# Optimization experiments

Measured on AMD Instinct MI355X. Metric: run time of the kernel, lower is better.

The kernel has to match this reference:

```python
import jax, jax.numpy as jnp
import numpy as np

D_MODEL, D_K, D_V, H_HEADS = 512, 64, 64, 8
HH, WW = 28, 28
LN_EPS = 1e-5


def setup_inputs() -> dict:
    key = jax.random.key(0)
    ks = jax.random.split(key, 20)
    b, nq, nk = 64, HH * WW, (HH // 2) * (WW // 2)
    def xavier(k, shape):
        fan_in, fan_out = shape[1], shape[0]
        std = float(np.sqrt(2.0 / (fan_in + fan_out)))
        return jax.random.normal(k, shape, jnp.float32) * std
    return {
        "queries": jax.random.normal(ks[0], (b, nq, D_MODEL), jnp.float32),
        "keys": jax.random.normal(ks[1], (b, nk, D_MODEL), jnp.float32),
        "values": jax.random.normal(ks[2], (b, nk, D_MODEL), jnp.float32),
        "Wq": xavier(ks[3], (H_HEADS * D_K, D_MODEL)), "bq": jnp.zeros((H_HEADS * D_K,), jnp.float32),
        "Wk": xavier(ks[4], (H_HEADS * D_K, D_MODEL)), "bk": jnp.zeros((H_HEADS * D_K,), jnp.float32),
        "Wv": xavier(ks[5], (H_HEADS * D_V, D_MODEL)), "bv": jnp.zeros((H_HEADS * D_V,), jnp.float32),
        "Wo": xavier(ks[6], (D_MODEL, H_HEADS * D_V)), "bo": jnp.zeros((D_MODEL,), jnp.float32),
        # depthwise 1x1 stride-2 conv: per-channel scale + bias
        "sr_w": xavier(ks[7], (D_MODEL, 1)).reshape(D_MODEL),
        "sr_b": jnp.zeros((D_MODEL,), jnp.float32),
        "ln_w": jnp.ones((D_MODEL,), jnp.float32), "ln_b": jnp.zeros((D_MODEL,), jnp.float32),
        # 1x1 conv mixing the head dim of attention scores
        "tw": xavier(ks[8], (H_HEADS, H_HEADS)), "tb": jnp.zeros((H_HEADS,), jnp.float32),
    }


def reference(queries, keys, values, Wq, bq, Wk, bk, Wv, bv, Wo, bo,
              sr_w, sr_b, ln_w, ln_b, tw, tb):
    b_s, nq, c = queries.shape
    # Q projection -> [b, h, nq, d_k]
    q = (jnp.einsum('bnc,oc->bno', queries, Wq) + bq).reshape(b_s, nq, H_HEADS, D_K).transpose(0, 2, 1, 3)
    # spatial reduction: depthwise 1x1 stride-2 conv == strided subsample * w + b
    x = queries.transpose(0, 2, 1).reshape(b_s, c, HH, WW)
    x = x[:, :, ::2, ::2] * sr_w[None, :, None, None] + sr_b[None, :, None, None]
    x = x.reshape(b_s, c, -1).transpose(0, 2, 1)  # [b, nk, c]
    # LayerNorm over channel dim
    mu = jnp.mean(x, axis=-1, keepdims=True)
    var = jnp.mean(jnp.square(x - mu), axis=-1, keepdims=True)
    x = (x - mu) * jax.lax.rsqrt(var + LN_EPS) * ln_w + ln_b
    nk = x.shape[1]
    k = (jnp.einsum('bnc,oc->bno', x, Wk) + bk).reshape(b_s, nk, H_HEADS, D_K)
    v = (jnp.einsum('bnc,oc->bno', x, Wv) + bv).reshape(b_s, nk, H_HEADS, D_V).transpose(0, 2, 1, 3)
    # attention scores [b, h, nq, nk]
    att = jnp.einsum('bhqd,bkhd->bhqk', q, k) / jnp.sqrt(jnp.float32(D_K))
    # transform: 1x1 conv across heads, then softmax over keys
    att = jnp.einsum('bhqk,gh->bgqk', att, tw) + tb[None, :, None, None]
    att = jax.nn.softmax(att, axis=-1)
    out = jnp.einsum('bhqk,bhkd->bhqd', att, v).transpose(0, 2, 1, 3).reshape(b_s, nq, H_HEADS * D_V)
    out = jnp.einsum('bno,co->bnc', out, Wo) + bo
    return out
```

## Files before the change

kernel.cpp:

```cpp
#include <hip/hip_runtime.h>
#include <stdint.h>

typedef unsigned short u16;
typedef unsigned int   u32;
typedef __attribute__((ext_vector_type(8))) __bf16 bf16x8;
typedef __attribute__((ext_vector_type(4))) float  f32x4;
typedef __attribute__((ext_vector_type(4))) short  s16x4;

#define NB  64
#define NQ  784
#define NK  196
#define NKP 208
#define DM  512

static __device__ inline u16 f2bf(float f) {
  u32 u = __float_as_uint(f);
  u32 r = (u + 0x7fffu + ((u >> 16) & 1u)) >> 16;
  return (u16)r;
}

static __device__ inline bf16x8 ld8(const u16* p) {
  return *reinterpret_cast<const bf16x8*>(p);
}
static __device__ inline f32x4 mfma16(bf16x8 a, bf16x8 b, f32x4 c) {
  return __builtin_amdgcn_mfma_f32_16x16x32_bf16(a, b, c, 0, 0, 0);
}
static __device__ inline f32x4 mfma16k16(s16x4 a, s16x4 b, f32x4 c) {
#if __has_builtin(__builtin_amdgcn_mfma_f32_16x16x16bf16_1k)
  return __builtin_amdgcn_mfma_f32_16x16x16bf16_1k(a, b, c, 0, 0, 0);
#elif __has_builtin(__builtin_amdgcn_mfma_f32_16x16x16_bf16)
  typedef __attribute__((ext_vector_type(4))) __bf16 bf16x4_t;
  union { s16x4 s; bf16x4_t b; } ua, ub;
  ua.s = a; ub.s = b;
  return __builtin_amdgcn_mfma_f32_16x16x16_bf16(ua.b, ub.b, c, 0, 0, 0);
#else
  asm volatile("v_mfma_f32_16x16x16_bf16 %0, %1, %2, %0\n\ts_nop 7\n\ts_nop 7"
               : "+v"(c) : "v"(a), "v"(b));
  return c;
#endif
}

static __device__ inline float sgpr_f(float x) {
  return __uint_as_float(__builtin_amdgcn_readfirstlane(__float_as_uint(x)));
}

static __device__ inline void gl_lds16(const void* g, void* l) {
  __builtin_amdgcn_global_load_lds(
      (const __attribute__((address_space(1))) void*)g,
      (__attribute__((address_space(3))) void*)l, 16, 0, 0);
}

__global__ __launch_bounds__(256) void cvt4_kernel(const float* __restrict__ Wq,
                                                   const float* __restrict__ Wk,
                                                   const float* __restrict__ Wv,
                                                   const float* __restrict__ Wo,
                                                   u16* __restrict__ oq,
                                                   u16* __restrict__ ok,
                                                   u16* __restrict__ ov,
                                                   u16* __restrict__ oo) {
  int sel = blockIdx.x >> 8;
  int blk = blockIdx.x & 255;
  const float* in = (sel == 0) ? Wq : (sel == 1) ? Wk : (sel == 2) ? Wv : Wo;
  u16* out = (sel == 0) ? oq : (sel == 1) ? ok : (sel == 2) ? ov : oo;
  int i = (blk * 256 + threadIdx.x) * 4;
  float4 f = *reinterpret_cast<const float4*>(in + i);
  ushort4 o;
  o.x = f2bf(f.x); o.y = f2bf(f.y); o.z = f2bf(f.z); o.w = f2bf(f.w);
  *reinterpret_cast<ushort4*>(out + i) = o;
}

__global__ __launch_bounds__(256) void cvtln_kernel(const float* __restrict__ q,
                                                    const float* __restrict__ sr_w,
                                                    const float* __restrict__ sr_b,
                                                    const float* __restrict__ ln_w,
                                                    const float* __restrict__ ln_b,
                                                    u16* __restrict__ qbf,
                                                    u16* __restrict__ xln) {
  int w = blockIdx.x * 4 + (threadIdx.x >> 6);
  int lane = threadIdx.x & 63;
  if (w >= NB * NQ) {
    int w2 = w - NB * NQ;
    if (w2 < NB * 12) {
      int b = w2 / 12, pr = w2 % 12;
      u16* outp = xln + ((size_t)(b * NKP + NK + pr)) * DM;
      *reinterpret_cast<uint4*>(outp + lane * 8) = make_uint4(0u, 0u, 0u, 0u);
    }
    return;
  }
  int b = w / NQ, n = w % NQ;
  const float* row = q + ((size_t)w) * DM;
  int c0 = lane * 4, c1 = 256 + lane * 4;
  float4 x0 = *reinterpret_cast<const float4*>(row + c0);
  float4 x1 = *reinterpret_cast<const float4*>(row + c1);
  u16* qp = qbf + (size_t)w * DM;
  ushort4 q0, q1;
  q0.x = f2bf(x0.x); q0.y = f2bf(x0.y); q0.z = f2bf(x0.z); q0.w = f2bf(x0.w);
  q1.x = f2bf(x1.x); q1.y = f2bf(x1.y); q1.z = f2bf(x1.z); q1.w = f2bf(x1.w);
  *reinterpret_cast<ushort4*>(qp + c0) = q0;
  *reinterpret_cast<ushort4*>(qp + c1) = q1;
  int y = n / 28, x = n % 28;
  if ((y & 1) | (x & 1)) return;
  int np = (y >> 1) * 14 + (x >> 1);
  float4 w0 = *reinterpret_cast<const float4*>(sr_w + c0);
  float4 w1 = *reinterpret_cast<const float4*>(sr_w + c1);
  float4 s0 = *reinterpret_cast<const float4*>(sr_b + c0);
  float4 s1 = *reinterpret_cast<const float4*>(sr_b + c1);
  float yv[8];
  yv[0] = x0.x * w0.x + s0.x; yv[1] = x0.y * w0.y + s0.y;
  yv[2] = x0.z * w0.z + s0.z; yv[3] = x0.w * w0.w + s0.w;
  yv[4] = x1.x * w1.x + s1.x; yv[5] = x1.y * w1.y + s1.y;
  yv[6] = x1.z * w1.z + s1.z; yv[7] = x1.w * w1.w + s1.w;
  float s = 0.f, ss = 0.f;
  #pragma unroll
  for (int i = 0; i < 8; i++) { s += yv[i]; ss += yv[i] * yv[i]; }
  #pragma unroll
  for (int off = 1; off < 64; off <<= 1) {
    s += __shfl_xor(s, off); ss += __shfl_xor(ss, off);
  }
  float mu = s * (1.f / 512.f);
  float var = ss * (1.f / 512.f) - mu * mu;
  float rs = rsqrtf(var + 1e-5f);
  float4 lw0 = *reinterpret_cast<const float4*>(ln_w + c0);
  float4 lw1 = *reinterpret_cast<const float4*>(ln_w + c1);
  float4 lb0 = *reinterpret_cast<const float4*>(ln_b + c0);
  float4 lb1 = *reinterpret_cast<const float4*>(ln_b + c1);
  ushort4 o0, o1;
  o0.x = f2bf((yv[0] - mu) * rs * lw0.x + lb0.x);
  o0.y = f2bf((yv[1] - mu) * rs * lw0.y + lb0.y);
  o0.z = f2bf((yv[2] - mu) * rs * lw0.z + lb0.z);
  o0.w = f2bf((yv[3] - mu) * rs * lw0.w + lb0.w);
  o1.x = f2bf((yv[4] - mu) * rs * lw1.x + lb1.x);
  o1.y = f2bf((yv[5] - mu) * rs * lw1.y + lb1.y);
  o1.z = f2bf((yv[6] - mu) * rs * lw1.z + lb1.z);
  o1.w = f2bf((yv[7] - mu) * rs * lw1.w + lb1.w);
  u16* outp = xln + ((size_t)(b * NKP + np)) * DM;
  *reinterpret_cast<ushort4*>(outp + c0) = o0;
  *reinterpret_cast<ushort4*>(outp + c1) = o1;
}

template <int OMODE>
static __device__ __forceinline__ void gemm_body(const u16* __restrict__ A,
                                                 const u16* __restrict__ Bw,
                                                 const float* __restrict__ bias,
                                                 void* __restrict__ Cptr,
                                                 int nt, int mt,
                                                 u16* Al0, u16* Al1,
                                                 u16* Bl0, u16* Bl1) {
  int wv = threadIdx.x >> 6, lane = threadIdx.x & 63;
  int lr = lane & 15, lg = lane >> 4;
  int wr = wv >> 1, wc = wv & 1;
  int row0 = mt * 128, col0 = nt * 128;

  auto stage = [&](int kk, int bi) {
    u16* Al = bi ? Al1 : Al0;
    u16* Bl = bi ? Bl1 : Bl0;
    #pragma unroll
    for (int i = 0; i < 4; i++) {
      int t = wv * 4 + i;
      int rr = (t & 7) * 16 + (lane >> 2);
      int cc = lane & 3;
      if (t < 8) {
        gl_lds16(A + (size_t)(row0 + rr) * DM + kk + cc * 8, (char*)Al + t * 1024);
      } else {
        gl_lds16(Bw + (size_t)(col0 + rr) * DM + kk + cc * 8, (char*)Bl + (t - 8) * 1024);
      }
    }
  };

  f32x4 acc[4][4] = {};
  stage(0, 0);
  __syncthreads();
  for (int s = 0; s < 16; s++) {
    int bi = s & 1;
    if (s < 15) stage((s + 1) * 32, bi ^ 1);
    u16* Al = bi ? Al1 : Al0;
    u16* Bl = bi ? Bl1 : Bl0;
    bf16x8 am[4], bn[4];
    #pragma unroll
    for (int m = 0; m < 4; m++)
      am[m] = ld8(Al + (wr * 64 + m * 16 + lr) * 32 + lg * 8);
    #pragma unroll
    for (int n = 0; n < 4; n++)
      bn[n] = ld8(Bl + (wc * 64 + n * 16 + lr) * 32 + lg * 8);
    #pragma unroll
    for (int m = 0; m < 4; m++)
      #pragma unroll
      for (int n = 0; n < 4; n++)
        acc[m][n] = mfma16(am[m], bn[n], acc[m][n]);
    __syncthreads();
  }
  if (OMODE == 2) {
    #pragma unroll
    for (int n = 0; n < 4; n++) {
      int col = col0 + wc * 64 + n * 16 + lr;
      float bs = bias[col];
      #pragma unroll
      for (int m = 0; m < 4; m++) {
        int rbase = row0 + wr * 64 + m * 16 + lg * 4;
        int bb = rbase / NKP;
        int kr = rbase % NKP;
        ushort4 o4;
        o4.x = f2bf(acc[m][n][0] + bs);
        o4.y = f2bf(acc[m][n][1] + bs);
        o4.z = f2bf(acc[m][n][2] + bs);
        o4.w = f2bf(acc[m][n][3] + bs);
        size_t dst = (((size_t)bb * 13 + (kr >> 4)) * 512 + col) * 16 + (kr & 15);
        *reinterpret_cast<ushort4*>(&((u16*)Cptr)[dst]) = o4;
      }
    }
  } else {
    #pragma unroll
    for (int n = 0; n < 4; n++) {
      int col = col0 + wc * 64 + n * 16 + lr;
      float bs = bias[col];
      #pragma unroll
      for (int m = 0; m < 4; m++) {
        #pragma unroll
        for (int r = 0; r < 4; r++) {
          int row = row0 + wr * 64 + m * 16 + lg * 4 + r;
          float v = acc[m][n][r] + bs;
          if (OMODE == 0) {
            ((u16*)Cptr)[(size_t)row * DM + col] = f2bf(v);
          } else {
            ((float*)Cptr)[(size_t)row * DM + col] = v;
          }
        }
      }
    }
  }
}

static __device__ inline void xcd_decode(int id, int& nt, int& mt) {
  nt = (id >> 3) & 3;
  mt = (id & 7) + 8 * (id >> 5);
}

__global__ __launch_bounds__(256) void qkvgemm_kernel(
    const u16* __restrict__ qbf, const u16* __restrict__ Wq,
    const float* __restrict__ bq, void* __restrict__ Qout,
    const u16* __restrict__ xln, const u16* __restrict__ Wk,
    const float* __restrict__ bk, void* __restrict__ Kout,
    const u16* __restrict__ Wv, const float* __restrict__ bv,
    void* __restrict__ Vout) {
  __shared__ __align__(16) u16 Al[2][128 * 32];
  __shared__ __align__(16) u16 Bl[2][128 * 32];
  int id = blockIdx.x;
  int nt, mt;
  if (id < 1568) {
    xcd_decode(id, nt, mt);
    gemm_body<0>(qbf, Wq, bq, Qout, nt, mt,
                 &Al[0][0], &Al[1][0], &Bl[0][0], &Bl[1][0]);
  } else if (id < 1984) {
    xcd_decode(id - 1568, nt, mt);
    gemm_body<0>(xln, Wk, bk, Kout, nt, mt,
                 &Al[0][0], &Al[1][0], &Bl[0][0], &Bl[1][0]);
  } else {
    xcd_decode(id - 1984, nt, mt);
    gemm_body<2>(xln, Wv, bv, Vout, nt, mt,
                 &Al[0][0], &Al[1][0], &Bl[0][0], &Bl[1][0]);
  }
}

__global__ __launch_bounds__(256) void ogemm_kernel(const u16* __restrict__ A,
                                                    const u16* __restrict__ Bw,
                                                    const float* __restrict__ bias,
                                                    void* __restrict__ Cptr) {
  __shared__ __align__(16) u16 Al[2][128 * 32];
  __shared__ __align__(16) u16 Bl[2][128 * 32];
  int nt, mt;
  xcd_decode(blockIdx.x, nt, mt);
  gemm_body<1>(A, Bw, bias, Cptr, nt, mt,
               &Al[0][0], &Al[1][0], &Bl[0][0], &Bl[1][0]);
}

__global__ __launch_bounds__(512) void attn_kernel(const u16* __restrict__ Q,
                                                   const u16* __restrict__ K,
                                                   const u16* __restrict__ VTt,
                                                   const float* __restrict__ tw,
                                                   u16* __restrict__ Oat) {
  __shared__ __align__(16) u16 Kl[16 * 512];
  __shared__ __align__(16) float s2[2][16 * 256];
  int i = blockIdx.x;
  int g8 = i & 7;
  int j = i >> 3;
  int qc = j % 25;
  int b = g8 + 8 * (j / 25);
  int tid = threadIdx.x, wv = tid >> 6, lane = tid & 63;
  int lr = lane & 15, lg = lane >> 4;
  int q0A = qc * 32;
  int q0B = (qc < 24) ? (q0A + 16) : q0A;

  const u16* Kb = K + (size_t)b * NKP * DM;
  const u16* Vtb = VTt + (size_t)b * 13 * 8192;

  float w0[8];
  #pragma unroll
  for (int h = 0; h < 8; h++)
    w0[h] = sgpr_f(tw[wv * 8 + h] * 0.125f);

  bf16x8 qr[2][2];
  #pragma unroll
  for (int t = 0; t < 2; t++) {
    const u16* Qb = Q + ((size_t)b * NQ + (t ? q0B : q0A)) * DM;
    qr[t][0] = ld8(Qb + (size_t)lr * DM + wv * 64 + lg * 8);
    qr[t][1] = ld8(Qb + (size_t)lr * DM + wv * 64 + 32 + lg * 8);
  }

  auto stageK = [&](int kt) {
    #pragma unroll
    for (int i2 = 0; i2 < 2; i2++) {
      int g = wv * 2 + i2;
      gl_lds16(Kb + (size_t)(kt * 16 + (lane & 15)) * DM + (g * 4 + (lane >> 4)) * 8,
               (char*)Kl + g * 1024);
    }
  };
  stageK(0);
  __syncthreads();

  f32x4 o[2][4] = {};
  float sumA = 0.f, sumB = 0.f;
  s16x4 vb[4];

  auto mixpv = [&](int ktm, int sbi) {
    bool masked = (ktm == 12) && (lg != 0);
    s16x4 pa[2];
    #pragma unroll
    for (int t = 0; t < 2; t++) {
      f32x4 sa = {0.f, 0.f, 0.f, 0.f};
      #pragma unroll
      for (int h = 0; h < 8; h++) {
        f32x4 scv = *reinterpret_cast<const f32x4*>(
            &s2[sbi][0] + (t * 8 + h) * 256 + lane * 4);
        sa += scv * w0[h];
      }
      float e0 = masked ? 0.f : __expf(sa[0]);
      float e1 = masked ? 0.f : __expf(sa[1]);
      float e2 = masked ? 0.f : __expf(sa[2]);
      float e3 = masked ? 0.f : __expf(sa[3]);
      if (t == 0) sumA += (e0 + e1) + (e2 + e3);
      else        sumB += (e0 + e1) + (e2 + e3);
      union { __bf16 e[4]; s16x4 sv; } pk;
      pk.e[0] = (__bf16)e0; pk.e[1] = (__bf16)e1;
      pk.e[2] = (__bf16)e2; pk.e[3] = (__bf16)e3;
      pa[t] = pk.sv;
    }
    __builtin_amdgcn_s_setprio(1);
    #pragma unroll
    for (int t = 0; t < 2; t++) {
      #pragma unroll
      for (int j2 = 0; j2 < 4; j2++)
        o[t][j2] = mfma16k16(pa[t], vb[j2], o[t][j2]);
    }
    __builtin_amdgcn_s_setprio(0);
  };

  for (int kt = 0; kt < 13; kt++) {
    int bi = kt & 1;

    if (kt > 0) {
      #pragma unroll
      for (int j2 = 0; j2 < 4; j2++) {
        int d = wv * 64 + j2 * 16 + lr;
        vb[j2] = *reinterpret_cast<const s16x4*>(
            Vtb + (size_t)(kt - 1) * 8192 + d * 16 + lg * 4);
      }
    }

    const u16* kbase = Kl + lg * 128 + lr * 8;
    __builtin_amdgcn_s_setprio(1);
    {
      bf16x8 kf0 = ld8(kbase + wv * 1024);
      bf16x8 kf1 = ld8(kbase + wv * 1024 + 512);
      #pragma unroll
      for (int t = 0; t < 2; t++) {
        f32x4 tt = {0.f, 0.f, 0.f, 0.f};
        tt = mfma16(kf0, qr[t][0], tt);
        tt = mfma16(kf1, qr[t][1], tt);
        *reinterpret_cast<f32x4*>(&s2[bi][0] + (t * 8 + wv) * 256 + lane * 4) = tt;
      }
    }
    __builtin_amdgcn_s_setprio(0);

    asm volatile("s_waitcnt lgkmcnt(0)" ::: "memory");
    __builtin_amdgcn_sched_barrier(0);
    if (kt < 12) stageK(kt + 1);

    if (kt > 0) mixpv(kt - 1, bi ^ 1);

    __syncthreads();
  }
  {
    #pragma unroll
    for (int j2 = 0; j2 < 4; j2++) {
      int d = wv * 64 + j2 * 16 + lr;
      vb[j2] = *reinterpret_cast<const s16x4*>(
          Vtb + (size_t)12 * 8192 + d * 16 + lg * 4);
    }
    mixpv(12, 0);
  }

  sumA += __shfl_xor(sumA, 16); sumA += __shfl_xor(sumA, 32);
  sumB += __shfl_xor(sumB, 16); sumB += __shfl_xor(sumB, 32);
  float ivA = 1.0f / sumA, ivB = 1.0f / sumB;
  #pragma unroll
  for (int t = 0; t < 2; t++) {
    if (t == 1 && qc == 24) break;
    int q0 = t ? q0B : q0A;
    float ivsrc = t ? ivB : ivA;
    #pragma unroll
    for (int r = 0; r < 4; r++) {
      int q = lg * 4 + r;
      float iv = __shfl(ivsrc, q);
      #pragma unroll
      for (int j2 = 0; j2 < 4; j2++) {
        Oat[((size_t)(b * NQ + q0 + q)) * DM + wv * 64 + j2 * 16 + lr] =
            f2bf(o[t][j2][r] * iv);
      }
    }
  }
}

extern "C" void kernel_launch(void* const* d_in, const int* in_sizes, int n_in,
                              void* d_out, int out_size, void* d_ws, size_t ws_size,
                              hipStream_t stream) {
  const float* queries = (const float*)d_in[0];
  const float* Wq = (const float*)d_in[3];
  const float* bq = (const float*)d_in[4];
  const float* Wk = (const float*)d_in[5];
  const float* bk = (const float*)d_in[6];
  const float* Wv = (const float*)d_in[7];
  const float* bv = (const float*)d_in[8];
  const float* Wo = (const float*)d_in[9];
  const float* bo = (const float*)d_in[10];
  const float* sr_w = (const float*)d_in[11];
  const float* sr_b = (const float*)d_in[12];
  const float* ln_w = (const float*)d_in[13];
  const float* ln_b = (const float*)d_in[14];
  const float* tw = (const float*)d_in[15];

  char* ws = (char*)d_ws;
  u16* wq_bf = (u16*)(ws + 0);
  u16* wk_bf = (u16*)(ws + 524288);
  u16* wv_bf = (u16*)(ws + 1048576);
  u16* wo_bf = (u16*)(ws + 1572864);
  u16* xln   = (u16*)(ws + 2097152);
  u16* Kbuf  = (u16*)(ws + 15728640);
  u16* VTt   = (u16*)(ws + 29360128);
  u16* Qbuf  = (u16*)(ws + 42991616);
  u16* qbf   = (u16*)(ws + 94371840);
  u16* Oat   = qbf;
  if (ws_size < 145752064u) return;

  cvt4_kernel<<<1024, 256, 0, stream>>>(Wq, Wk, Wv, Wo,
                                        wq_bf, wk_bf, wv_bf, wo_bf);

  cvtln_kernel<<<(NB * NQ + NB * 12 + 3) / 4, 256, 0, stream>>>(
      queries, sr_w, sr_b, ln_w, ln_b, qbf, xln);

  qkvgemm_kernel<<<2400, 256, 0, stream>>>(qbf, wq_bf, bq, Qbuf,
                                           xln, wk_bf, bk, Kbuf,
                                           wv_bf, bv, VTt);

  attn_kernel<<<dim3(1600), 512, 0, stream>>>(Qbuf, Kbuf, VTt, tw, Oat);

  ogemm_kernel<<<1568, 256, 0, stream>>>(Oat, wo_bf, bo, d_out);
}
```

Baseline: 234.0 us.

## Fuse fp32-to-bf16 query conversion into Q projection GEMM A-load

The separate pass that converted every query row to bf16 is removed, and the LayerNorm kernel now processes only the subsampled rows. A new Q GEMM kernel loads fp32 activations directly into registers, converts them to bf16 and writes them to LDS while double-buffering, which avoids writing and re-reading a 51 MB intermediate. The fused QKV launch is split into separate Q and KV launches, so the Q GEMM and the KV GEMMs no longer share one grid. The register-staged A path may hide latency less well than the direct global-to-LDS loads used before.

```diff
diff --git a/kernel.cpp b/kernel.cpp
--- a/kernel.cpp
+++ b/kernel.cpp
@@ -69,17 +69,16 @@
   *reinterpret_cast<ushort4*>(out + i) = o;
 }
 
-__global__ __launch_bounds__(256) void cvtln_kernel(const float* __restrict__ q,
-                                                    const float* __restrict__ sr_w,
-                                                    const float* __restrict__ sr_b,
-                                                    const float* __restrict__ ln_w,
-                                                    const float* __restrict__ ln_b,
-                                                    u16* __restrict__ qbf,
-                                                    u16* __restrict__ xln) {
+__global__ __launch_bounds__(256) void ln_kernel(const float* __restrict__ q,
+                                                 const float* __restrict__ sr_w,
+                                                 const float* __restrict__ sr_b,
+                                                 const float* __restrict__ ln_w,
+                                                 const float* __restrict__ ln_b,
+                                                 u16* __restrict__ xln) {
   int w = blockIdx.x * 4 + (threadIdx.x >> 6);
   int lane = threadIdx.x & 63;
-  if (w >= NB * NQ) {
-    int w2 = w - NB * NQ;
+  if (w >= NB * NK) {
+    int w2 = w - NB * NK;
     if (w2 < NB * 12) {
       int b = w2 / 12, pr = w2 % 12;
       u16* outp = xln + ((size_t)(b * NKP + NK + pr)) * DM;
@@ -87,20 +86,12 @@
     }
     return;
   }
-  int b = w / NQ, n = w % NQ;
-  const float* row = q + ((size_t)w) * DM;
+  int b = w / NK, np = w % NK;
+  int src_n = (2 * (np / 14)) * 28 + 2 * (np % 14);
+  const float* row = q + ((size_t)(b * NQ + src_n)) * DM;
   int c0 = lane * 4, c1 = 256 + lane * 4;
   float4 x0 = *reinterpret_cast<const float4*>(row + c0);
   float4 x1 = *reinterpret_cast<const float4*>(row + c1);
-  u16* qp = qbf + (size_t)w * DM;
-  ushort4 q0, q1;
-  q0.x = f2bf(x0.x); q0.y = f2bf(x0.y); q0.z = f2bf(x0.z); q0.w = f2bf(x0.w);
-  q1.x = f2bf(x1.x); q1.y = f2bf(x1.y); q1.z = f2bf(x1.z); q1.w = f2bf(x1.w);
-  *reinterpret_cast<ushort4*>(qp + c0) = q0;
-  *reinterpret_cast<ushort4*>(qp + c1) = q1;
-  int y = n / 28, x = n % 28;
-  if ((y & 1) | (x & 1)) return;
-  int np = (y >> 1) * 14 + (x >> 1);
   float4 w0 = *reinterpret_cast<const float4*>(sr_w + c0);
   float4 w1 = *reinterpret_cast<const float4*>(sr_w + c1);
   float4 s0 = *reinterpret_cast<const float4*>(sr_b + c0);
@@ -235,27 +226,101 @@
   mt = (id & 7) + 8 * (id >> 5);
 }
 
-__global__ __launch_bounds__(256) void qkvgemm_kernel(
-    const u16* __restrict__ qbf, const u16* __restrict__ Wq,
-    const float* __restrict__ bq, void* __restrict__ Qout,
-    const u16* __restrict__ xln, const u16* __restrict__ Wk,
-    const float* __restrict__ bk, void* __restrict__ Kout,
-    const u16* __restrict__ Wv, const float* __restrict__ bv,
-    void* __restrict__ Vout) {
+__global__ __launch_bounds__(256) void qgemm_kernel(const float* __restrict__ A,
+                                                    const u16* __restrict__ Bw,
+                                                    const float* __restrict__ bias,
+                                                    u16* __restrict__ Cptr) {
+  __shared__ __align__(16) u16 Al[2][128 * 32];
+  __shared__ __align__(16) u16 Bl[2][128 * 32];
+  int nt, mt;
+  xcd_decode(blockIdx.x, nt, mt);
+  int wv = threadIdx.x >> 6, lane = threadIdx.x & 63;
+  int lr = lane & 15, lg = lane >> 4;
+  int wr = wv >> 1, wc = wv & 1;
+  int row0 = mt * 128, col0 = nt * 128;
+  int arow = threadIdx.x >> 1, ahalf = threadIdx.x & 1;
+  const float* asrc = A + (size_t)(row0 + arow) * DM + ahalf * 16;
+
+  float4 ar[4];
+  auto loadA = [&](int kk) {
+    #pragma unroll
+    for (int i = 0; i < 4; i++)
+      ar[i] = *reinterpret_cast<const float4*>(asrc + kk + i * 4);
+  };
+  auto writeA = [&](u16* Alw) {
+    union { u16 s[16]; uint4 u[2]; } pk;
+    const float* f = reinterpret_cast<const float*>(ar);
+    #pragma unroll
+    for (int i = 0; i < 16; i++) pk.s[i] = f2bf(f[i]);
+    *reinterpret_cast<uint4*>(Alw + arow * 32 + ahalf * 16) = pk.u[0];
+    *reinterpret_cast<uint4*>(Alw + arow * 32 + ahalf * 16 + 8) = pk.u[1];
+  };
+  auto stageB = [&](int kk, u16* Blw) {
+    #pragma unroll
+    for (int i = 0; i < 2; i++) {
+      int t = wv * 2 + i;
+      gl_lds16(Bw + (size_t)(col0 + t * 16 + (lane >> 2)) * DM + kk + (lane & 3) * 8,
+               (char*)Blw + t * 1024);
+    }
+  };
+
+  f32x4 acc[4][4] = {};
+  loadA(0); writeA(&Al[0][0]); stageB(0, &Bl[0][0]);
+  __syncthreads();
+  for (int s = 0; s < 16; s++) {
+    int bi = s & 1;
+    u16* Alc = &Al[bi][0];
+    u16* Blc = &Bl[bi][0];
+    u16* Aln = &Al[bi ^ 1][0];
+    u16* Bln = &Bl[bi ^ 1][0];
+    if (s < 15) { loadA((s + 1) * 32); stageB((s + 1) * 32, Bln); }
+    bf16x8 am[4], bn[4];
+    #pragma unroll
+    for (int m = 0; m < 4; m++)
+      am[m] = ld8(Alc + (wr * 64 + m * 16 + lr) * 32 + lg * 8);
+    #pragma unroll
+    for (int n = 0; n < 4; n++)
+      bn[n] = ld8(Blc + (wc * 64 + n * 16 + lr) * 32 + lg * 8);
+    #pragma unroll
+    for (int m = 0; m < 4; m++)
+      #pragma unroll
+      for (int n = 0; n < 4; n++)
+        acc[m][n] = mfma16(am[m], bn[n], acc[m][n]);
+    if (s < 15) writeA(Aln);
+    __syncthreads();
+  }
+  #pragma unroll
+  for (int n = 0; n < 4; n++) {
+    int col = col0 + wc * 64 + n * 16 + lr;
+    float bs = bias[col];
+    #pragma unroll
+    for (int m = 0; m < 4; m++) {
+      #pragma unroll
+      for (int r = 0; r < 4; r++) {
+        int row = row0 + wr * 64 + m * 16 + lg * 4 + r;
+        Cptr[(size_t)row * DM + col] = f2bf(acc[m][n][r] + bs);
+      }
+    }
+  }
+}
+
+__global__ __launch_bounds__(256) void kvgemm_kernel(const u16* __restrict__ xln,
+                                                     const u16* __restrict__ Wk,
+                                                     const float* __restrict__ bk,
+                                                     void* __restrict__ Kout,
+                                                     const u16* __restrict__ Wv,
+                                                     const float* __restrict__ bv,
+                                                     void* __restrict__ Vout) {
   __shared__ __align__(16) u16 Al[2][128 * 32];
   __shared__ __align__(16) u16 Bl[2][128 * 32];
   int id = blockIdx.x;
   int nt, mt;
-  if (id < 1568) {
+  if (id < 416) {
     xcd_decode(id, nt, mt);
-    gemm_body<0>(qbf, Wq, bq, Qout, nt, mt,
-                 &Al[0][0], &Al[1][0], &Bl[0][0], &Bl[1][0]);
-  } else if (id < 1984) {
-    xcd_decode(id - 1568, nt, mt);
     gemm_body<0>(xln, Wk, bk, Kout, nt, mt,
                  &Al[0][0], &Al[1][0], &Bl[0][0], &Bl[1][0]);
   } else {
-    xcd_decode(id - 1984, nt, mt);
+    xcd_decode(id - 416, nt, mt);
     gemm_body<2>(xln, Wv, bv, Vout, nt, mt,
                  &Al[0][0], &Al[1][0], &Bl[0][0], &Bl[1][0]);
   }
@@ -447,19 +512,18 @@
   u16* Kbuf  = (u16*)(ws + 15728640);
   u16* VTt   = (u16*)(ws + 29360128);
   u16* Qbuf  = (u16*)(ws + 42991616);
-  u16* qbf   = (u16*)(ws + 94371840);
-  u16* Oat   = qbf;
+  u16* Oat   = (u16*)(ws + 94371840);
   if (ws_size < 145752064u) return;
 
   cvt4_kernel<<<1024, 256, 0, stream>>>(Wq, Wk, Wv, Wo,
                                         wq_bf, wk_bf, wv_bf, wo_bf);
 
-  cvtln_kernel<<<(NB * NQ + NB * 12 + 3) / 4, 256, 0, stream>>>(
-      queries, sr_w, sr_b, ln_w, ln_b, qbf, xln);
-
-  qkvgemm_kernel<<<2400, 256, 0, stream>>>(qbf, wq_bf, bq, Qbuf,
-                                           xln, wk_bf, bk, Kbuf,
-                                           wv_bf, bv, VTt);
+  ln_kernel<<<(NB * NK + NB * 12 + 3) / 4, 256, 0, stream>>>(
+      queries, sr_w, sr_b, ln_w, ln_b, xln);
+
+  qgemm_kernel<<<1568, 256, 0, stream>>>(queries, wq_bf, bq, Qbuf);
+  kvgemm_kernel<<<832, 256, 0, stream>>>(xln, wk_bf, bk, Kbuf,
+                                         wv_bf, bv, VTt);
 
   attn_kernel<<<dim3(1600), 512, 0, stream>>>(Qbuf, Kbuf, VTt, tw, Oat);
 
```

New measurement: 258.9 us. 1.11x slower.
